# Kernel tuning notes

Measured on AMD Instinct MI355X. Metric: run time of the kernel, lower is better.

Reference implementation:

```python
import jax, jax.numpy as jnp
import numpy as np


def setup_inputs() -> dict:
    key = jax.random.key(0)
    kx, ky = jax.random.split(key)
    x = jax.random.normal(kx, (4, 8192, 3), dtype=jnp.float32)
    y = jax.random.normal(ky, (4, 8192, 3), dtype=jnp.float32)
    return {"x": x, "y": y}


def _chamfer(x, y):
    # x: [B, N, D], y: [B, M, D]
    x2 = jnp.sum(x * x, axis=-1)                      # [B, N]
    y2 = jnp.sum(y * y, axis=-1)                      # [B, M]
    xy = jnp.einsum("bnd,bmd->bnm", x, y)             # [B, N, M]
    d2 = x2[:, :, None] + y2[:, None, :] - 2.0 * xy   # [B, N, M]
    d2 = jnp.maximum(d2, 0.0)
    cham_x = jnp.min(d2, axis=2).mean(axis=1)         # [B] min over M, mean over N
    cham_y = jnp.min(d2, axis=1).mean(axis=1)         # [B] min over N, mean over M
    return cham_x + cham_y                            # [B]


def reference(x, y):
    per_batch = _chamfer(x, y)
    return jnp.mean(per_batch)  # batch_reduction='mean'
```

## Files before the change

### kernel.cpp

```cpp
#include <hip/hip_runtime.h>


#define N_      8192
#define RPB     4096
#define FLT_BIG 3.0e38f

typedef float v2f __attribute__((ext_vector_type(2)));

__global__ void zero_out_kernel(float* out) { *out = 0.0f; }

static __device__ __forceinline__ float rot16(float v) {
    return __uint_as_float((unsigned)__builtin_amdgcn_update_dpp(
        0, (int)__float_as_uint(v), 0x121, 0xf, 0xf, true));
}
static __device__ __forceinline__ v2f rot16v(v2f v) {
    v2f r; r.x = rot16(v.x); r.y = rot16(v.y); return r;
}

static __device__ __forceinline__ void do_record_sym(
    v2f pxs, v2f pys, v2f pzs, v2f wv,
    const v2f* qx, const v2f* qy, const v2f* qz, const v2f* qnv,
    float* acc, v2f* cacc)
{
    #pragma unroll
    for (int j = 0; j < 4; ++j) {
        v2f td, ts;
        asm("v_pk_fma_f32 %0, %1, %2, %3"
            : "=v"(td) : "v"(qz[j]), "v"(pzs), "v"(wv));
        asm("v_pk_fma_f32 %0, %1, %2, %3 op_sel:[0,1,1] op_sel_hi:[1,0,0]"
            : "=v"(ts) : "v"(qz[j]), "v"(pzs), "v"(wv));
        asm("v_pk_fma_f32 %0, %1, %2, %0"
            : "+v"(td) : "v"(qy[j]), "v"(pys));
        asm("v_pk_fma_f32 %0, %1, %2, %0 op_sel:[0,1,0] op_sel_hi:[1,0,1]"
            : "+v"(ts) : "v"(qy[j]), "v"(pys));
        asm("v_pk_fma_f32 %0, %1, %2, %0"
            : "+v"(td) : "v"(qx[j]), "v"(pxs));
        asm("v_pk_fma_f32 %0, %1, %2, %0 op_sel:[0,1,0] op_sel_hi:[1,0,1]"
            : "+v"(ts) : "v"(qx[j]), "v"(pxs));
        asm("v_min3_f32 %0, %0, %1, %2" : "+v"(acc[2*j])   : "v"(td.x), "v"(ts.x));
        asm("v_min3_f32 %0, %0, %1, %2" : "+v"(acc[2*j+1]) : "v"(td.y), "v"(ts.y));
        v2f tdq, tsq;
        asm("v_pk_add_f32 %0, %1, %2" : "=v"(tdq) : "v"(td), "v"(qnv[j]));
        asm("v_pk_add_f32 %0, %1, %2" : "=v"(tsq) : "v"(ts), "v"(qnv[j]));
        asm("v_min3_f32 %0, %0, %1, %2" : "+v"(cacc->x) : "v"(tdq.x), "v"(tsq.y));
        asm("v_min3_f32 %0, %0, %1, %2" : "+v"(cacc->y) : "v"(tsq.x), "v"(tdq.y));
    }
}

__global__ __launch_bounds__(512, 4) void chamfer_kernel(
    const float* __restrict__ xraw, const float* __restrict__ yraw,
    unsigned int* __restrict__ pmin)
{
    __shared__ float red[8 * 512];
    __shared__ float colbuf[8][128];

    const int tid  = threadIdx.x;
    const int lane = tid & 63;
    const int wave = __builtin_amdgcn_readfirstlane(tid >> 6);
    const int blk  = blockIdx.x;
    const int batch = blk >> 7;
    const int qg    = (blk >> 3) & 15;
    const int seg   = blk & 7;

    const int qbase = batch * N_ + qg * 512;
    float f[24];
    {
        const float4* qv = (const float4*)(xraw + (size_t)qbase * 3) + lane * 6;
        #pragma unroll
        for (int k = 0; k < 6; ++k) {
            float4 t = qv[k];
            f[4*k] = t.x; f[4*k+1] = t.y; f[4*k+2] = t.z; f[4*k+3] = t.w;
        }
    }
    v2f qx[4], qy[4], qz[4], qnv[4];
    float acc[8];
    #pragma unroll
    for (int j = 0; j < 4; ++j) {
        qnv[j].x = fmaf(f[6*j+0], f[6*j+0],
                   fmaf(f[6*j+1], f[6*j+1], f[6*j+2] * f[6*j+2]));
        qnv[j].y = fmaf(f[6*j+3], f[6*j+3],
                   fmaf(f[6*j+4], f[6*j+4], f[6*j+5] * f[6*j+5]));
        qx[j] = (v2f){-2.0f * f[6*j+0], -2.0f * f[6*j+3]};
        qy[j] = (v2f){-2.0f * f[6*j+1], -2.0f * f[6*j+4]};
        qz[j] = (v2f){-2.0f * f[6*j+2], -2.0f * f[6*j+5]};
        acc[2*j] = FLT_BIG; acc[2*j+1] = FLT_BIG;
    }

    const int rbase = seg * 512 + wave * 64;
    const float2* rp = (const float2*)
        (yraw + (size_t)(batch * RPB + rbase + (lane & 15)) * 6);
    float2 A = rp[0], Bv = rp[1], Cv = rp[2];
    #pragma unroll 1
    for (int fl = 0; fl < 4; ++fl) {
        v2f pxs = (v2f){A.x,  Bv.y};
        v2f pys = (v2f){A.y,  Cv.x};
        v2f pzs = (v2f){Bv.x, Cv.y};
        v2f wv;
        wv.x = fmaf(A.x,  A.x,  fmaf(A.y,  A.y,  Bv.x * Bv.x));
        wv.y = fmaf(Bv.y, Bv.y, fmaf(Cv.x, Cv.x, Cv.y * Cv.y));
        if (fl < 3) {
            const float2* np = rp + (fl + 1) * 48;
            A = np[0]; Bv = np[1]; Cv = np[2];
        }
        v2f cacc = (v2f){FLT_BIG, FLT_BIG};
        #pragma unroll
        for (int s = 0; s < 16; ++s) {
            if (s) {
                pxs = rot16v(pxs); pys = rot16v(pys);
                pzs = rot16v(pzs); wv  = rot16v(wv);
                cacc = rot16v(cacc);
            }
            do_record_sym(pxs, pys, pzs, wv, qx, qy, qz, qnv, acc, &cacc);
        }
        cacc = rot16v(cacc);
        cacc.x = fminf(cacc.x, __shfl_xor(cacc.x, 16));
        cacc.x = fminf(cacc.x, __shfl_xor(cacc.x, 32));
        cacc.y = fminf(cacc.y, __shfl_xor(cacc.y, 16));
        cacc.y = fminf(cacc.y, __shfl_xor(cacc.y, 32));
        if (lane < 16) {
            colbuf[wave][fl * 32 + lane * 2]     = fmaxf(0.0f, cacc.x);
            colbuf[wave][fl * 32 + lane * 2 + 1] = fmaxf(0.0f, cacc.y);
        }
    }

    {
        unsigned int* py = pmin + 32768 + batch * N_ + 2 * rbase;
        #pragma unroll
        for (int k = 0; k < 2; ++k) {
            int idx = lane * 2 + k;
            float v = colbuf[wave][idx];
            atomicMin(&py[idx], __float_as_uint(v));
        }
    }

    #pragma unroll
    for (int j = 0; j < 8; ++j) red[wave * 512 + lane * 8 + j] = acc[j];
    __syncthreads();
    float m = red[tid];
    #pragma unroll
    for (int w = 1; w < 8; ++w) m = fminf(m, red[w * 512 + tid]);
    int gq = qbase + tid;
    float ax = xraw[gq*3+0], ay = xraw[gq*3+1], az = xraw[gq*3+2];
    float qn = fmaf(ax, ax, fmaf(ay, ay, az * az));
    float d2 = fmaxf(0.0f, qn + m);
    atomicMin(&pmin[gq], __float_as_uint(d2));
}

__global__ __launch_bounds__(256) void sum_kernel(
    const unsigned int* __restrict__ pmin, float* __restrict__ out)
{
    int i = blockIdx.x * 256 + threadIdx.x;
    float4 v = ((const float4*)pmin)[i];
    float s = v.x + v.y + v.z + v.w;
    #pragma unroll
    for (int off = 32; off > 0; off >>= 1) s += __shfl_xor(s, off);
    if ((threadIdx.x & 63) == 0) atomicAdd(out, s * (1.0f / 32768.0f));
}

__global__ __launch_bounds__(1024) void chamfer_raw_kernel(
    const float* __restrict__ xraw, const float* __restrict__ yraw,
    float* __restrict__ out)
{
    __shared__ float4 red4[16][64];
    const int tid  = threadIdx.x;
    const int wave = tid >> 6;
    const int lane = tid & 63;
    const int blk  = blockIdx.x;
    const bool xdir = (blk < 128);
    const int b    = (blk & 127) >> 5;
    const int qofs = (blk & 31) << 8;
    const float* qraw = xdir ? xraw : yraw;
    const float* oraw = xdir ? yraw : xraw;
    float qx0[4], qx1[4], qx2[4], acc[4];
    #pragma unroll
    for (int q = 0; q < 4; ++q) {
        int gq = b * N_ + qofs + lane*4 + q;
        qx0[q] = qraw[gq*3+0]; qx1[q] = qraw[gq*3+1]; qx2[q] = qraw[gq*3+2];
        acc[q] = FLT_BIG;
    }
    const float* opp = oraw + (size_t)(b * N_ + wave * 512) * 3;
    #pragma unroll 4
    for (int k = 0; k < 512; ++k) {
        float p0 = opp[k*3+0], p1 = opp[k*3+1], p2 = opp[k*3+2];
        float w  = fmaf(p0, p0, fmaf(p1, p1, p2*p2));
        #pragma unroll
        for (int q = 0; q < 4; ++q) {
            float dot = qx0[q]*p0 + qx1[q]*p1 + qx2[q]*p2;
            acc[q] = fminf(acc[q], fmaf(-2.0f, dot, w));
        }
    }
    red4[wave][lane] = make_float4(acc[0], acc[1], acc[2], acc[3]);
    __syncthreads();
    if (tid < 256) {
        const float* red = (const float*)red4;
        float m = red[tid];
        #pragma unroll
        for (int w = 1; w < 16; ++w) m = fminf(m, red[w*256 + tid]);
        int gq = b * N_ + qofs + tid;
        float ax = qraw[gq*3+0], ay = qraw[gq*3+1], az = qraw[gq*3+2];
        float d2 = fmaxf(0.0f, fmaf(ax,ax,fmaf(ay,ay,az*az)) + m);
        #pragma unroll
        for (int off = 32; off > 0; off >>= 1) d2 += __shfl_xor(d2, off);
        if ((tid & 63) == 0) atomicAdd(out, d2 * (1.0f / 32768.0f));
    }
}

extern "C" void kernel_launch(void* const* d_in, const int* in_sizes, int n_in,
                              void* d_out, int out_size, void* d_ws, size_t ws_size,
                              hipStream_t stream)
{
    const float* x = (const float*)d_in[0];
    const float* y = (const float*)d_in[1];
    float* out = (float*)d_out;

    const size_t need = (size_t)65536 * 4;
    if (ws_size >= need) {
        unsigned int* pmin = (unsigned int*)d_ws;
        hipMemsetAsync(pmin, 0xFF, need, stream);
        hipMemsetAsync(out, 0, 4, stream);
        chamfer_kernel<<<512, 512, 0, stream>>>(x, y, pmin);
        sum_kernel<<<64, 256, 0, stream>>>(pmin, out);
    } else {
        zero_out_kernel<<<1, 1, 0, stream>>>(out);
        chamfer_raw_kernel<<<256, 1024, 0, stream>>>(x, y, out);
    }
}
```

Baseline: 92.90 us.

## Replace atomicMin partials and memsets with per-segment partial buffers

The main kernel now writes per-segment row minima and per-query-group column minima into separate plain workspace slices instead of doing atomicMin into a pre-filled buffer. This removes both hipMemsetAsync calls, and the output is zeroed inside the main kernel. The sum kernel now reduces across the 8 row partials and 16 column partials before summing. The cost is a larger workspace and more reads in the final reduction. The output zeroing happens in the first kernel and the atomicAdds only run in the second, so the ordering is safe.

Result: slower. 100.5 us (+8.2%).

```diff
diff --git a/kernel.cpp b/kernel.cpp
--- a/kernel.cpp
+++ b/kernel.cpp
@@ -49,7 +49,9 @@
 
 __global__ __launch_bounds__(512, 4) void chamfer_kernel(
     const float* __restrict__ xraw, const float* __restrict__ yraw,
-    unsigned int* __restrict__ pmin)
+    float* __restrict__ rowpart,
+    float* __restrict__ colpart,
+    float* __restrict__ out)
 {
     __shared__ float red[8 * 512];
     __shared__ float colbuf[8][128];
@@ -61,6 +63,8 @@
     const int batch = blk >> 7;
     const int qg    = (blk >> 3) & 15;
     const int seg   = blk & 7;
+
+    if (blk == 0 && tid == 0) *out = 0.0f;
 
     const int qbase = batch * N_ + qg * 512;
     float f[24];
@@ -124,13 +128,9 @@
     }
 
     {
-        unsigned int* py = pmin + 32768 + batch * N_ + 2 * rbase;
-        #pragma unroll
-        for (int k = 0; k < 2; ++k) {
-            int idx = lane * 2 + k;
-            float v = colbuf[wave][idx];
-            atomicMin(&py[idx], __float_as_uint(v));
-        }
+        float2* cp = (float2*)(colpart + (size_t)qg * 32768 + batch * N_ + 2 * rbase);
+        float2 v = ((const float2*)colbuf[wave])[lane];
+        cp[lane] = v;
     }
 
     #pragma unroll
@@ -139,22 +139,35 @@
     float m = red[tid];
     #pragma unroll
     for (int w = 1; w < 8; ++w) m = fminf(m, red[w * 512 + tid]);
-    int gq = qbase + tid;
-    float ax = xraw[gq*3+0], ay = xraw[gq*3+1], az = xraw[gq*3+2];
-    float qn = fmaf(ax, ax, fmaf(ay, ay, az * az));
-    float d2 = fmaxf(0.0f, qn + m);
-    atomicMin(&pmin[gq], __float_as_uint(d2));
-}
-
-__global__ __launch_bounds__(256) void sum_kernel(
-    const unsigned int* __restrict__ pmin, float* __restrict__ out)
-{
-    int i = blockIdx.x * 256 + threadIdx.x;
-    float4 v = ((const float4*)pmin)[i];
-    float s = v.x + v.y + v.z + v.w;
-    #pragma unroll
-    for (int off = 32; off > 0; off >>= 1) s += __shfl_xor(s, off);
-    if ((threadIdx.x & 63) == 0) atomicAdd(out, s * (1.0f / 32768.0f));
+    rowpart[(size_t)seg * 32768 + qbase + tid] = m;
+}
+
+__global__ __launch_bounds__(512) void sum_kernel(
+    const float* __restrict__ xraw,
+    const float* __restrict__ rowpart, const float* __restrict__ colpart,
+    float* __restrict__ out)
+{
+    const int b   = blockIdx.x;
+    const int tid = threadIdx.x;
+    float d2;
+    if (b < 64) {
+        int gq = b * 512 + tid;
+        float m = rowpart[gq];
+        #pragma unroll
+        for (int s = 1; s < 8; ++s) m = fminf(m, rowpart[(size_t)s * 32768 + gq]);
+        float ax = xraw[gq*3+0], ay = xraw[gq*3+1], az = xraw[gq*3+2];
+        float qn = fmaf(ax, ax, fmaf(ay, ay, az * az));
+        d2 = fmaxf(0.0f, qn + m);
+    } else {
+        int gp = (b - 64) * 512 + tid;
+        float m = colpart[gp];
+        #pragma unroll
+        for (int q = 1; q < 16; ++q) m = fminf(m, colpart[(size_t)q * 32768 + gp]);
+        d2 = m;
+    }
+    #pragma unroll
+    for (int off = 32; off > 0; off >>= 1) d2 += __shfl_xor(d2, off);
+    if ((tid & 63) == 0) atomicAdd(out, d2 * (1.0f / 32768.0f));
 }
 
 __global__ __launch_bounds__(1024) void chamfer_raw_kernel(
@@ -213,13 +226,12 @@
     const float* y = (const float*)d_in[1];
     float* out = (float*)d_out;
 
-    const size_t need = (size_t)65536 * 4;
+    const size_t need = (size_t)(8 + 16) * 32768 * sizeof(float);
     if (ws_size >= need) {
-        unsigned int* pmin = (unsigned int*)d_ws;
-        hipMemsetAsync(pmin, 0xFF, need, stream);
-        hipMemsetAsync(out, 0, 4, stream);
-        chamfer_kernel<<<512, 512, 0, stream>>>(x, y, pmin);
-        sum_kernel<<<64, 256, 0, stream>>>(pmin, out);
+        float* rowpart = (float*)d_ws;
+        float* colpart = rowpart + (size_t)8 * 32768;
+        chamfer_kernel<<<512, 512, 0, stream>>>(x, y, rowpart, colpart, out);
+        sum_kernel<<<128, 512, 0, stream>>>(x, rowpart, colpart, out);
     } else {
         zero_out_kernel<<<1, 1, 0, stream>>>(out);
         chamfer_raw_kernel<<<256, 1024, 0, stream>>>(x, y, out);
```
